# Optimization experiments

Measured on AMD Instinct MI355X. Metric: run time of the kernel, lower is better.

## Reference

```python
import jax, jax.numpy as jnp
import numpy as np

DIM = 1024
EXP = 4           # expansion_factor
NUM_EXPERTS = 4
BATCH, SEQ = 4, 4096


def setup_inputs() -> dict:
    key = jax.random.key(0)
    ks = jax.random.split(key, 6)
    x = jax.random.normal(ks[0], (BATCH, SEQ, DIM), dtype=jnp.float32)
    token_mask = jax.random.randint(ks[1], (BATCH, SEQ), 0, NUM_EXPERTS, dtype=jnp.int32)
    hid = DIM * EXP
    s1 = 1.0 / np.sqrt(DIM)
    s2 = 1.0 / np.sqrt(hid)
    # nn.Linear layout: weight [out_features, in_features]
    w1 = jax.random.uniform(ks[2], (hid, DIM), minval=-s1, maxval=s1, dtype=jnp.float32)
    b1 = jax.random.uniform(ks[3], (hid,), minval=-s1, maxval=s1, dtype=jnp.float32)
    w2 = jax.random.uniform(ks[4], (DIM, hid), minval=-s2, maxval=s2, dtype=jnp.float32)
    b2 = jax.random.uniform(ks[5], (DIM,), minval=-s2, maxval=s2, dtype=jnp.float32)
    return {"x": x, "w1": w1, "b1": b1, "w2": w2, "b2": b2, "token_mask": token_mask}


def _nested_ffn(x, w1, b1, w2, b2, token_mask):
    dim = x.shape[-1]            # in_features of proj1
    out_dim = w2.shape[0]        # out_features of proj2 (== dim)
    # Expert m uses the first D_m = width >> (E-1-m) features (matryoshka nesting).
    # Expand (proj1): truncating input features to D_m and doing a full GEMM is
    # exactly equivalent to zeroing features >= D_m, so we mask then do one GEMM.
    d_in = dim >> (NUM_EXPERTS - 1 - token_mask)             # [B,S]
    in_mask = jnp.arange(dim) < d_in[..., None]              # [B,S,dim]
    h = jnp.einsum('bsd,fd->bsf', jnp.where(in_mask, x, jnp.zeros((), x.dtype)), w1) + b1
    h = jax.nn.gelu(h, approximate=False)                    # torch nn.GELU() default = erf
    # Contract (proj2): expert m produces only the first D_m outputs (incl. bias),
    # padded with zeros -> compute full GEMM then mask outputs.
    d_out = out_dim >> (NUM_EXPERTS - 1 - token_mask)        # [B,S]
    out_mask = jnp.arange(out_dim) < d_out[..., None]        # [B,S,out_dim]
    y = jnp.einsum('bsf,df->bsd', h, w2) + b2
    return jnp.where(out_mask, y, jnp.zeros((), y.dtype))


def reference(x, w1, b1, w2, b2, token_mask):
    return _nested_ffn(x, w1, b1, w2, b2, token_mask)
```

## Files before the change

### kernel.cpp

```cpp
#include <hip/hip_runtime.h>
#include <hip/hip_bf16.h>


typedef __bf16 bf16x8 __attribute__((ext_vector_type(8)));
typedef float f32x4 __attribute__((ext_vector_type(4)));

#define M_TOK   16384
#define DIM     1024
#define HID     4096

#define META_TK    40
#define META_BLK   64
#define META_BLK2  192
#define META_MAP   256
#define META_RT    2560

__device__ inline unsigned int pk_bf16(float a, float b) {
  unsigned int r;
  asm("v_cvt_pk_bf16_f32 %0, %1, %2" : "=v"(r) : "v"(a), "v"(b));
  return r;
}

__device__ inline float gelu_f(float v) {
  float v2 = v * v;
  float w = v * fmaf(0.10294324f, v2, 2.30220830f);
  float e = __builtin_amdgcn_exp2f(-w);
  return v * __builtin_amdgcn_rcpf(1.0f + e);
}

__device__ inline void async_copy16(const void* g, void* s) {
  __builtin_amdgcn_global_load_lds(
      (const __attribute__((address_space(1))) unsigned int*)g,
      (__attribute__((address_space(3))) unsigned int*)s,
      16, 0, 0);
}

template<int ROWS, int LDK, int THREADS>
__device__ inline void stage_tile(const unsigned short* __restrict__ g,
                                  int row0, int k0, char* lds) {
  const char* gbase = (const char*)g;
  int tid = threadIdx.x;
#pragma unroll
  for (int i = 0; i < ROWS * 8 / THREADS; ++i) {
    int q = i * THREADS + tid;
    int r = q >> 3;
    int c = q & 7;
    int gc = c ^ (r & 7);
    const void* gp = gbase + ((size_t)(row0 + r) * LDK + (size_t)k0 + gc * 8) * 2;
    async_copy16(gp, lds + (size_t)q * 16);
  }
}

__global__ __launch_bounds__(1024) void sortw_kernel(
    const int* __restrict__ tm,
    const float* __restrict__ w1,
    const float* __restrict__ w2,
    int* __restrict__ meta,
    unsigned short* __restrict__ w1b,
    unsigned short* __restrict__ w2b) {
  int tid = threadIdx.x;
  if (blockIdx.x != 0) {
    size_t i = (size_t)(blockIdx.x - 1) * 4096 + tid * 4;
    const float* src;
    unsigned short* dst;
    if (i < (size_t)HID * DIM) { src = w1; dst = w1b; }
    else { src = w2 - (size_t)HID * DIM; dst = w2b - (size_t)HID * DIM; }
    float4 v = *(const float4*)(src + i);
    uint2 o;
    o.x = pk_bf16(v.x, v.y);
    o.y = pk_bf16(v.z, v.w);
    *(uint2*)(dst + i) = o;
    return;
  }

  __shared__ unsigned short rt[16384];
  __shared__ unsigned int w01[16], w23[16];
  __shared__ int sbase[4];
  __shared__ int cb[128];
  int lane = tid & 63, wv = tid >> 6;

  int c0 = 0, c1 = 0, c2 = 0, c3 = 0;
  unsigned int epack = 0;
  int4 tv[4];
#pragma unroll
  for (int j = 0; j < 4; ++j)
    tv[j] = *(const int4*)(tm + tid * 16 + j * 4);
#pragma unroll
  for (int j = 0; j < 4; ++j) {
    int e;
    e = tv[j].x; epack |= (unsigned)e << (2 * (4 * j + 0)); c0 += (e == 0); c1 += (e == 1); c2 += (e == 2); c3 += (e == 3);
    e = tv[j].y; epack |= (unsigned)e << (2 * (4 * j + 1)); c0 += (e == 0); c1 += (e == 1); c2 += (e == 2); c3 += (e == 3);
    e = tv[j].z; epack |= (unsigned)e << (2 * (4 * j + 2)); c0 += (e == 0); c1 += (e == 1); c2 += (e == 2); c3 += (e == 3);
    e = tv[j].w; epack |= (unsigned)e << (2 * (4 * j + 3)); c0 += (e == 0); c1 += (e == 1); c2 += (e == 2); c3 += (e == 3);
  }
  unsigned int p01 = (unsigned)c0 | ((unsigned)c1 << 16);
  unsigned int p23 = (unsigned)c2 | ((unsigned)c3 << 16);
  unsigned int i01 = p01, i23 = p23;
#pragma unroll
  for (int s = 1; s < 64; s <<= 1) {
    unsigned int t0 = __shfl_up(i01, s, 64);
    unsigned int t1 = __shfl_up(i23, s, 64);
    if (lane >= s) { i01 += t0; i23 += t1; }
  }
  if (lane == 63) { w01[wv] = i01; w23[wv] = i23; }
  unsigned int e01 = i01 - p01, e23 = i23 - p23;
  __syncthreads();
  if (tid < 16) {
    unsigned int a = w01[tid], b = w23[tid];
    unsigned int ia = a, ib = b;
#pragma unroll
    for (int s = 1; s < 16; s <<= 1) {
      unsigned int t0 = __shfl_up(ia, s, 64);
      unsigned int t1 = __shfl_up(ib, s, 64);
      if (tid >= s) { ia += t0; ib += t1; }
    }
    w01[tid] = ia - a;
    w23[tid] = ib - b;
    if (tid == 15) {
      int t0 = (int)(ia & 0xFFFF), t1 = (int)(ia >> 16), t2 = (int)(ib & 0xFFFF);
      sbase[0] = 0; sbase[1] = t0; sbase[2] = t0 + t1; sbase[3] = t0 + t1 + t2;
    }
  }
  __syncthreads();
  int off0 = sbase[0] + (int)((w01[wv] & 0xFFFF) + (e01 & 0xFFFF));
  int off1 = sbase[1] + (int)((w01[wv] >> 16) + (e01 >> 16));
  int off2 = sbase[2] + (int)((w23[wv] & 0xFFFF) + (e23 & 0xFFFF));
  int off3 = sbase[3] + (int)((w23[wv] >> 16) + (e23 >> 16));
#pragma unroll
  for (int j = 0; j < 16; ++j) {
    int e = (epack >> (2 * j)) & 3;
    int t = tid * 16 + j;
    int pos = (e == 0) ? off0++ : (e == 1) ? off1++ : (e == 2) ? off2++ : off3++;
    rt[pos] = (unsigned short)(t | (e << 14));
  }
  __syncthreads();

  if (tid < 128) {
    int last = tid * 128 + 127;
    int e = (last >= sbase[1]) + (last >= sbase[2]) + (last >= sbase[3]);
    cb[tid] = 1 << e;
    meta[META_BLK + tid] = 128 << e;
  }
  if (tid < 64) {
    int last = tid * 256 + 255;
    int e = (last >= sbase[1]) + (last >= sbase[2]) + (last >= sbase[3]);
    meta[META_BLK2 + tid] = 128 << e;
  }
  __syncthreads();
  if (tid < 8) {
    int k = tid;
    int* map = meta + META_MAP + k * 128;
    int Tk = 0;
    for (int j = 0; j < 16; ++j) Tk += cb[k + 8 * j];
    meta[META_TK + k] = Tk;
    int pos = 0, zpos = Tk;
    for (int j = 0; j < 16; ++j) {
      int s = k + 8 * j;
      int n = cb[s];
      for (int c = 0; c < n; ++c) map[pos++] = s * 8 + c;
      for (int c = n; c < 8; ++c) map[zpos++] = s * 8 + c;
    }
  }
  int* rowtok = meta + META_RT;
#pragma unroll
  for (int j = 0; j < 16; ++j)
    rowtok[j * 1024 + tid] = (int)rt[j * 1024 + tid];
}

__global__ void prepx_kernel(const float* __restrict__ x,
                             const int* __restrict__ meta,
                             unsigned short* __restrict__ xb) {
  int b = blockIdx.x;
  int tid = threadIdx.x;
  int mt = meta[META_RT + b];
  int t = mt & 0x3FFF;
  int din = 128 << (mt >> 14);
  int kb = meta[META_BLK2 + (b >> 8)];
  int d = tid * 4;
  if (d < kb) {
    uint2 o; o.x = 0; o.y = 0;
    if (d < din) {
      float4 v = *(const float4*)(x + (size_t)t * DIM + d);
      o.x = pk_bf16(v.x, v.y);
      o.y = pk_bf16(v.z, v.w);
    }
    *(uint2*)(xb + (size_t)b * DIM + d) = o;
  }
}

__global__ __launch_bounds__(512, 1) void gemm1_kernel(
    const unsigned short* __restrict__ A,
    const unsigned short* __restrict__ B,
    const float* __restrict__ bias,
    const int* __restrict__ meta,
    unsigned short* __restrict__ H)
{
  constexpr int K = DIM, N = HID;
  __shared__ char smem[131072];
  int tid = threadIdx.x;
  int lane = tid & 63, quad = lane >> 4, l15 = lane & 15;
  int wave = tid >> 6;
  int wm = wave >> 2, wn = wave & 3;
  int Bk = blockIdx.x & 7, ord = blockIdx.x >> 3;
  int rowblk = 63 - (ord >> 1);
  int row0 = rowblk * 256, col0 = (Bk * 2 + (ord & 1)) * 256;
  int kmax = meta[META_BLK2 + rowblk];

  int chb = (quad ^ (l15 & 7)) << 4;

  f32x4 acc[8][4] = {};

  stage_tile<256, K, 512>(A, row0, 0, smem);
  stage_tile<256, K, 512>(B, col0, 0, smem + 32768);

  int nt = kmax >> 6;
  for (int t = 0; t < nt; ++t) {
    char* buf = smem + ((t & 1) << 16);
    if (t + 1 < nt) {
      char* nbuf = smem + (((t + 1) & 1) << 16);
      int kn = (t + 1) << 6;
      stage_tile<256, K, 512>(A, row0, kn, nbuf);
      stage_tile<256, K, 512>(B, col0, kn, nbuf + 32768);
      asm volatile("s_waitcnt vmcnt(8)" ::: "memory");
    } else {
      asm volatile("s_waitcnt vmcnt(0)" ::: "memory");
    }
    __builtin_amdgcn_s_barrier();
    char* As = buf;
    char* Bs = buf + 32768;
    bf16x8 bg[4][2];
#pragma unroll
    for (int nf = 0; nf < 4; ++nf)
#pragma unroll
      for (int kk = 0; kk < 2; ++kk)
        bg[nf][kk] = *(const bf16x8*)(Bs + (wn * 64 + nf * 16 + l15) * 128 + (chb ^ (kk << 6)));
    __builtin_amdgcn_s_setprio(1);
#pragma unroll
    for (int mf = 0; mf < 8; ++mf) {
      bf16x8 a0 = *(const bf16x8*)(As + (wm * 128 + mf * 16 + l15) * 128 + chb);
      bf16x8 a1 = *(const bf16x8*)(As + (wm * 128 + mf * 16 + l15) * 128 + (chb ^ 64));
#pragma unroll
      for (int nf = 0; nf < 4; ++nf)
        acc[mf][nf] = __builtin_amdgcn_mfma_f32_16x16x32_bf16(
            bg[nf][0], a0, acc[mf][nf], 0, 0, 0);
#pragma unroll
      for (int nf = 0; nf < 4; ++nf)
        acc[mf][nf] = __builtin_amdgcn_mfma_f32_16x16x32_bf16(
            bg[nf][1], a1, acc[mf][nf], 0, 0, 0);
    }
    __builtin_amdgcn_s_setprio(0);
    __builtin_amdgcn_s_barrier();
  }

  int t_base = row0 + wm * 128;
  int f_base = col0 + wn * 64;
#pragma unroll
  for (int nf = 0; nf < 4; ++nf) {
    int f0 = f_base + nf * 16 + quad * 4;
    float4 bv = *(const float4*)(bias + f0);
#pragma unroll
    for (int mf = 0; mf < 8; ++mf) {
      int t = t_base + mf * 16 + l15;
      float v0 = gelu_f(acc[mf][nf][0] + bv.x);
      float v1 = gelu_f(acc[mf][nf][1] + bv.y);
      float v2 = gelu_f(acc[mf][nf][2] + bv.z);
      float v3 = gelu_f(acc[mf][nf][3] + bv.w);
      uint2 p;
      p.x = pk_bf16(v0, v1);
      p.y = pk_bf16(v2, v3);
      *(uint2*)(H + (size_t)t * N + f0) = p;
    }
  }
}

__global__ __launch_bounds__(256) void gemm2_kernel(
    const unsigned short* __restrict__ A,
    const unsigned short* __restrict__ B,
    const float* __restrict__ bias,
    const int* __restrict__ meta,
    float* __restrict__ out)
{
  constexpr int K = HID, N = DIM;
  int Bk = blockIdx.x & 7, ord = blockIdx.x >> 3;
  int Tk = meta[META_TK + Bk];
  int mp = meta[META_MAP + Bk * 128 + ord];
  int row0 = (mp >> 3) * 128, col0 = (mp & 7) * 128;
  const int* rowtok = meta + META_RT;
  int tid = threadIdx.x;

  if (ord >= Tk) {
    float4 z = make_float4(0.f, 0.f, 0.f, 0.f);
#pragma unroll
    for (int i = 0; i < 16; ++i) {
      int idx = i * 256 + tid;
      int r = idx >> 5;
      int col = (idx & 31) * 4;
      int t = rowtok[row0 + r] & 0x3FFF;
      *(float4*)(out + (size_t)t * N + col0 + col) = z;
    }
    return;
  }

  __shared__ char smem[65536];
  int lane = tid & 63, quad = lane >> 4, l15 = lane & 15;
  int wave = tid >> 6, wm = wave & 1, wn = wave >> 1;
  int chb = (quad ^ (l15 & 7)) << 4;

  f32x4 acc[4][4] = {};

  stage_tile<128, K, 256>(A, row0, 0, smem);
  stage_tile<128, K, 256>(B, col0, 0, smem + 16384);

  constexpr int NT = K >> 6;
  for (int t = 0; t < NT; ++t) {
    char* buf = smem + ((t & 1) << 15);
    if (t + 1 < NT) {
      char* nbuf = smem + (((t + 1) & 1) << 15);
      int kn = (t + 1) << 6;
      stage_tile<128, K, 256>(A, row0, kn, nbuf);
      stage_tile<128, K, 256>(B, col0, kn, nbuf + 16384);
      asm volatile("s_waitcnt vmcnt(8)" ::: "memory");
    } else {
      asm volatile("s_waitcnt vmcnt(0)" ::: "memory");
    }
    __builtin_amdgcn_s_barrier();
    char* As = buf;
    char* Bs = buf + 16384;
#pragma unroll
    for (int kk = 0; kk < 2; ++kk) {
      int xo = chb ^ (kk << 6);
      bf16x8 bg[4];
#pragma unroll
      for (int nt2 = 0; nt2 < 4; ++nt2)
        bg[nt2] = *(const bf16x8*)(Bs + (wn * 64 + nt2 * 16 + l15) * 128 + xo);
#pragma unroll
      for (int mt = 0; mt < 4; ++mt) {
        bf16x8 am = *(const bf16x8*)(As + (wm * 64 + mt * 16 + l15) * 128 + xo);
#pragma unroll
        for (int nt2 = 0; nt2 < 4; ++nt2)
          acc[mt][nt2] = __builtin_amdgcn_mfma_f32_16x16x32_bf16(
              bg[nt2], am, acc[mt][nt2], 0, 0, 0);
      }
    }
    __builtin_amdgcn_s_barrier();
  }

  int p_base = row0 + wm * 64;
  int d_base = col0 + wn * 64;
  float4 bv[4];
#pragma unroll
  for (int nt2 = 0; nt2 < 4; ++nt2)
    bv[nt2] = *(const float4*)(bias + d_base + nt2 * 16 + quad * 4);
#pragma unroll
  for (int mt = 0; mt < 4; ++mt) {
    int m2 = rowtok[p_base + mt * 16 + l15];
    int t = m2 & 0x3FFF;
    int dout = 128 << (m2 >> 14);
#pragma unroll
    for (int nt2 = 0; nt2 < 4; ++nt2) {
      int d0 = d_base + nt2 * 16 + quad * 4;
      bool ok = d0 < dout;
      float4 o;
      o.x = ok ? acc[mt][nt2][0] + bv[nt2].x : 0.0f;
      o.y = ok ? acc[mt][nt2][1] + bv[nt2].y : 0.0f;
      o.z = ok ? acc[mt][nt2][2] + bv[nt2].z : 0.0f;
      o.w = ok ? acc[mt][nt2][3] + bv[nt2].w : 0.0f;
      *(float4*)(out + (size_t)t * N + d0) = o;
    }
  }
}

extern "C" void kernel_launch(void* const* d_in, const int* in_sizes, int n_in,
                              void* d_out, int out_size, void* d_ws, size_t ws_size,
                              hipStream_t stream) {
  const float* x  = (const float*)d_in[0];
  const float* w1 = (const float*)d_in[1];
  const float* b1 = (const float*)d_in[2];
  const float* w2 = (const float*)d_in[3];
  const float* b2 = (const float*)d_in[4];
  const int*   tm = (const int*)d_in[5];
  float* out = (float*)d_out;

  char* ws = (char*)d_ws;
  int* meta = (int*)ws;
  unsigned short* xb  = (unsigned short*)(ws + 131072);
  unsigned short* w1b = (unsigned short*)(ws + 33685504);
  unsigned short* w2b = (unsigned short*)(ws + 42074112);
  unsigned short* hb  = (unsigned short*)(ws + 50462720);

  sortw_kernel<<<2049, 1024, 0, stream>>>(tm, w1, w2, meta, w1b, w2b);
  prepx_kernel<<<M_TOK, 256, 0, stream>>>(x, meta, xb);
  gemm1_kernel<<<1024, 512, 0, stream>>>(xb, w1b, b1, meta, hb);
  gemm2_kernel<<<1024, 256, 0, stream>>>(hb, w2b, b2, meta, out);
}
```

Baseline: 327.3 us.

## Use 1024-thread blocks in gemm1 with 16 waves of 64x64 sub-tiles

Doubles the gemm1 workgroup from 8 to 16 waves, shrinking each wave's output tile from 128x64 to 64x64 and halving its accumulator registers. Staging loads are spread over more threads and the wait count is adjusted. The aim is more latency hiding per CU, at the cost of fewer MFMAs per LDS fragment load and more barrier participants.

```diff
diff --git a/kernel.cpp b/kernel.cpp
--- a/kernel.cpp
+++ b/kernel.cpp
@@ -188,7 +188,7 @@
   }
 }
 
-__global__ __launch_bounds__(512, 1) void gemm1_kernel(
+__global__ __launch_bounds__(1024, 4) void gemm1_kernel(
     const unsigned short* __restrict__ A,
     const unsigned short* __restrict__ B,
     const float* __restrict__ bias,
@@ -208,10 +208,10 @@
 
   int chb = (quad ^ (l15 & 7)) << 4;
 
-  f32x4 acc[8][4] = {};
-
-  stage_tile<256, K, 512>(A, row0, 0, smem);
-  stage_tile<256, K, 512>(B, col0, 0, smem + 32768);
+  f32x4 acc[4][4] = {};
+
+  stage_tile<256, K, 1024>(A, row0, 0, smem);
+  stage_tile<256, K, 1024>(B, col0, 0, smem + 32768);
 
   int nt = kmax >> 6;
   for (int t = 0; t < nt; ++t) {
@@ -219,52 +219,50 @@
     if (t + 1 < nt) {
       char* nbuf = smem + (((t + 1) & 1) << 16);
       int kn = (t + 1) << 6;
-      stage_tile<256, K, 512>(A, row0, kn, nbuf);
-      stage_tile<256, K, 512>(B, col0, kn, nbuf + 32768);
-      asm volatile("s_waitcnt vmcnt(8)" ::: "memory");
+      stage_tile<256, K, 1024>(A, row0, kn, nbuf);
+      stage_tile<256, K, 1024>(B, col0, kn, nbuf + 32768);
+      asm volatile("s_waitcnt vmcnt(4)" ::: "memory");
     } else {
       asm volatile("s_waitcnt vmcnt(0)" ::: "memory");
     }
     __builtin_amdgcn_s_barrier();
     char* As = buf;
     char* Bs = buf + 32768;
-    bf16x8 bg[4][2];
-#pragma unroll
-    for (int nf = 0; nf < 4; ++nf)
-#pragma unroll
-      for (int kk = 0; kk < 2; ++kk)
-        bg[nf][kk] = *(const bf16x8*)(Bs + (wn * 64 + nf * 16 + l15) * 128 + (chb ^ (kk << 6)));
     __builtin_amdgcn_s_setprio(1);
 #pragma unroll
-    for (int mf = 0; mf < 8; ++mf) {
-      bf16x8 a0 = *(const bf16x8*)(As + (wm * 128 + mf * 16 + l15) * 128 + chb);
-      bf16x8 a1 = *(const bf16x8*)(As + (wm * 128 + mf * 16 + l15) * 128 + (chb ^ 64));
+    for (int kk = 0; kk < 2; ++kk) {
+      int xo = chb ^ (kk << 6);
+      bf16x8 af[4], bg[4];
+#pragma unroll
+      for (int mt = 0; mt < 4; ++mt)
+        af[mt] = *(const bf16x8*)(As + (wm * 64 + mt * 16 + l15) * 128 + xo);
 #pragma unroll
       for (int nf = 0; nf < 4; ++nf)
-        acc[mf][nf] = __builtin_amdgcn_mfma_f32_16x16x32_bf16(
-            bg[nf][0], a0, acc[mf][nf], 0, 0, 0);
-#pragma unroll
-      for (int nf = 0; nf < 4; ++nf)
-        acc[mf][nf] = __builtin_amdgcn_mfma_f32_16x16x32_bf16(
-            bg[nf][1], a1, acc[mf][nf], 0, 0, 0);
+        bg[nf] = *(const bf16x8*)(Bs + (wn * 64 + nf * 16 + l15) * 128 + xo);
+#pragma unroll
+      for (int mt = 0; mt < 4; ++mt)
+#pragma unroll
+        for (int nf = 0; nf < 4; ++nf)
+          acc[mt][nf] = __builtin_amdgcn_mfma_f32_16x16x32_bf16(
+              bg[nf], af[mt], acc[mt][nf], 0, 0, 0);
     }
     __builtin_amdgcn_s_setprio(0);
     __builtin_amdgcn_s_barrier();
   }
 
-  int t_base = row0 + wm * 128;
+  int t_base = row0 + wm * 64;
   int f_base = col0 + wn * 64;
 #pragma unroll
   for (int nf = 0; nf < 4; ++nf) {
     int f0 = f_base + nf * 16 + quad * 4;
     float4 bv = *(const float4*)(bias + f0);
 #pragma unroll
-    for (int mf = 0; mf < 8; ++mf) {
-      int t = t_base + mf * 16 + l15;
-      float v0 = gelu_f(acc[mf][nf][0] + bv.x);
-      float v1 = gelu_f(acc[mf][nf][1] + bv.y);
-      float v2 = gelu_f(acc[mf][nf][2] + bv.z);
-      float v3 = gelu_f(acc[mf][nf][3] + bv.w);
+    for (int mt = 0; mt < 4; ++mt) {
+      int t = t_base + mt * 16 + l15;
+      float v0 = gelu_f(acc[mt][nf][0] + bv.x);
+      float v1 = gelu_f(acc[mt][nf][1] + bv.y);
+      float v2 = gelu_f(acc[mt][nf][2] + bv.z);
+      float v3 = gelu_f(acc[mt][nf][3] + bv.w);
       uint2 p;
       p.x = pk_bf16(v0, v1);
       p.y = pk_bf16(v2, v3);
@@ -390,6 +388,6 @@
 
   sortw_kernel<<<2049, 1024, 0, stream>>>(tm, w1, w2, meta, w1b, w2b);
   prepx_kernel<<<M_TOK, 256, 0, stream>>>(x, meta, xb);
-  gemm1_kernel<<<1024, 512, 0, stream>>>(xb, w1b, b1, meta, hb);
+  gemm1_kernel<<<1024, 1024, 0, stream>>>(xb, w1b, b1, meta, hb);
   gemm2_kernel<<<1024, 256, 0, stream>>>(hb, w2b, b2, meta, out);
 }
```

After: 317.6 us. -3.0%, faster.
